# Optimization experiments

Measured on AMD Instinct MI355X. Metric: run time of the kernel, lower is better.

Reference implementation:

```python
import jax, jax.numpy as jnp
import numpy as np

NUM_CLASS = 8192
FEAT_DIM = 512
BATCH = 131072


def setup_inputs() -> dict:
    key = jax.random.key(0)
    k1, k2, k3 = jax.random.split(key, 3)
    batch_samples = jax.random.normal(k1, (BATCH, FEAT_DIM), dtype=jnp.float32)
    class_sums = jnp.zeros((NUM_CLASS, FEAT_DIM), dtype=jnp.float32)
    targets = jax.random.randint(k2, (BATCH,), 0, NUM_CLASS, dtype=jnp.int64)
    idx = jax.random.randint(k3, (BATCH,), 0, BATCH, dtype=jnp.int64)
    return {"batch_samples": batch_samples, "class_sums": class_sums,
            "targets": targets, "idx": idx}


def reference(batch_samples, class_sums, targets, idx):
    # Original forward: for each unique label, class_sums[label] += sum of rows
    # of batch_samples with that label. This is exactly a segment-sum
    # (scatter-add by class label) accumulated into class_sums.
    # idx is unused in the forward math (kept for signature fidelity).
    inc = jax.ops.segment_sum(batch_samples, targets, num_segments=NUM_CLASS)
    return class_sums + inc  # updated class_sums buffer [num_class, feat_dim]
```

## Files before the change

### kernel.cpp

```cpp
#include <hip/hip_runtime.h>
#include <hip/hip_bf16.h>


#define FEAT 512
#define FEAT4 128
#define SCAN_THREADS 256

typedef float f4 __attribute__((ext_vector_type(4)));

__global__ void k_hist(const int4* __restrict__ t4, int* __restrict__ counts,
                       int n4, const int* __restrict__ targets, int batch) {
    int i = blockIdx.x * blockDim.x + threadIdx.x;
    if (i < n4) {
        int4 v = t4[i];
        atomicAdd(&counts[v.x], 1);
        atomicAdd(&counts[v.y], 1);
        atomicAdd(&counts[v.z], 1);
        atomicAdd(&counts[v.w], 1);
    }
    if (i == 0) {
        for (int k = n4 * 4; k < batch; ++k) atomicAdd(&counts[targets[k]], 1);
    }
}

__global__ __launch_bounds__(SCAN_THREADS) void k_scan(const int* __restrict__ counts,
                                                       int* __restrict__ fill,
                                                       int num_class) {
    __shared__ int sh[8192 + 256];
    __shared__ int sums[SCAN_THREADS];
    const int t = threadIdx.x;
    const int bins = num_class / SCAN_THREADS;

    for (int i = t; i < num_class; i += SCAN_THREADS) sh[i + (i >> 5)] = counts[i];
    __syncthreads();

    const int base = t * bins;
    int s = 0;
    for (int i = 0; i < bins; ++i) { int idx = base + i; s += sh[idx + (idx >> 5)]; }
    sums[t] = s;
    __syncthreads();
    for (int off = 1; off < SCAN_THREADS; off <<= 1) {
        int v = (t >= off) ? sums[t - off] : 0;
        __syncthreads();
        sums[t] += v;
        __syncthreads();
    }
    int run = sums[t] - s;
    for (int i = 0; i < bins; ++i) {
        int idx = base + i;
        int c = sh[idx + (idx >> 5)];
        sh[idx + (idx >> 5)] = run;
        run += c;
    }
    __syncthreads();
    for (int i = t; i < num_class; i += SCAN_THREADS) fill[i] = sh[i + (i >> 5)];
}

__global__ void k_scatter(const int4* __restrict__ t4, int* __restrict__ fill,
                          int* __restrict__ rows, int n4,
                          const int* __restrict__ targets, int batch) {
    int i = blockIdx.x * blockDim.x + threadIdx.x;
    if (i < n4) {
        int4 v = t4[i];
        int r = i * 4;
        rows[atomicAdd(&fill[v.x], 1)] = r + 0;
        rows[atomicAdd(&fill[v.y], 1)] = r + 1;
        rows[atomicAdd(&fill[v.z], 1)] = r + 2;
        rows[atomicAdd(&fill[v.w], 1)] = r + 3;
    }
    if (i == 0) {
        for (int k = n4 * 4; k < batch; ++k)
            rows[atomicAdd(&fill[targets[k]], 1)] = k;
    }
}

__global__ __launch_bounds__(128) void k_sum(const f4* __restrict__ batch,
                                             const f4* __restrict__ csums,
                                             const int* __restrict__ fill,
                                             const int* __restrict__ counts,
                                             const int* __restrict__ rows,
                                             f4* __restrict__ out) {
    const int c = blockIdx.x;
    const int t = threadIdx.x;
    const int n = counts[c];
    const int start = fill[c] - n;

    f4 acc = csums[(size_t)c * FEAT4 + t];

    __shared__ int sidx[512];
    for (int chunk = 0; chunk < n; chunk += 512) {
        const int m = min(n - chunk, 512);
        for (int j = t; j < m; j += 128) sidx[j] = rows[start + chunk + j];
        __syncthreads();

        int j = 0;
        for (; j + 8 <= m; j += 8) {
            f4 v0 = __builtin_nontemporal_load(&batch[(size_t)sidx[j + 0] * FEAT4 + t]);
            f4 v1 = __builtin_nontemporal_load(&batch[(size_t)sidx[j + 1] * FEAT4 + t]);
            f4 v2 = __builtin_nontemporal_load(&batch[(size_t)sidx[j + 2] * FEAT4 + t]);
            f4 v3 = __builtin_nontemporal_load(&batch[(size_t)sidx[j + 3] * FEAT4 + t]);
            f4 v4 = __builtin_nontemporal_load(&batch[(size_t)sidx[j + 4] * FEAT4 + t]);
            f4 v5 = __builtin_nontemporal_load(&batch[(size_t)sidx[j + 5] * FEAT4 + t]);
            f4 v6 = __builtin_nontemporal_load(&batch[(size_t)sidx[j + 6] * FEAT4 + t]);
            f4 v7 = __builtin_nontemporal_load(&batch[(size_t)sidx[j + 7] * FEAT4 + t]);
            acc += ((v0 + v1) + (v2 + v3)) + ((v4 + v5) + (v6 + v7));
        }
        for (; j < m; ++j) {
            f4 v = __builtin_nontemporal_load(&batch[(size_t)sidx[j] * FEAT4 + t]);
            acc += v;
        }
        __syncthreads();
    }
    __builtin_nontemporal_store(acc, &out[(size_t)c * FEAT4 + t]);
}

__global__ void k_copy(const float4* __restrict__ src, float4* __restrict__ dst, int n4) {
    int i = blockIdx.x * blockDim.x + threadIdx.x;
    if (i < n4) dst[i] = src[i];
}

__global__ __launch_bounds__(128) void k_atomic(const float4* __restrict__ batch,
                                                const int* __restrict__ targets,
                                                float* __restrict__ out, int batch_n) {
    const int r = blockIdx.x;
    const int t = threadIdx.x;
    if (r >= batch_n) return;
    float4 v = batch[(size_t)r * FEAT4 + t];
    float* o = out + (size_t)targets[r] * FEAT + t * 4;
    atomicAdd(o + 0, v.x);
    atomicAdd(o + 1, v.y);
    atomicAdd(o + 2, v.z);
    atomicAdd(o + 3, v.w);
}

extern "C" void kernel_launch(void* const* d_in, const int* in_sizes, int n_in,
                              void* d_out, int out_size, void* d_ws, size_t ws_size,
                              hipStream_t stream) {
    const float* batch_samples = (const float*)d_in[0];
    const float* class_sums    = (const float*)d_in[1];
    const int*   targets       = (const int*)d_in[2];

    const int batch     = in_sizes[2];
    const int num_class = out_size / FEAT;
    float* out = (float*)d_out;

    const size_t need = (size_t)num_class * 4 * 2 + (size_t)batch * 4;
    if (ws_size >= need && (num_class % SCAN_THREADS) == 0 && num_class <= 8192) {
        int* counts = (int*)d_ws;
        int* fill   = counts + num_class;
        int* rows   = fill + num_class;
        const int n4 = batch / 4;

        (void)hipMemsetAsync(counts, 0, (size_t)num_class * 4, stream);
        k_hist<<<(n4 + 255) / 256, 256, 0, stream>>>((const int4*)targets, counts,
                                                     n4, targets, batch);
        k_scan<<<1, SCAN_THREADS, 0, stream>>>(counts, fill, num_class);
        k_scatter<<<(n4 + 255) / 256, 256, 0, stream>>>((const int4*)targets, fill,
                                                        rows, n4, targets, batch);
        k_sum<<<num_class, 128, 0, stream>>>((const f4*)batch_samples,
                                             (const f4*)class_sums,
                                             fill, counts, rows,
                                             (f4*)out);
    } else {
        const int nv4 = out_size / 4;
        k_copy<<<(nv4 + 255) / 256, 256, 0, stream>>>((const float4*)class_sums,
                                                      (float4*)out, nv4);
        k_atomic<<<batch, 128, 0, stream>>>((const float4*)batch_samples,
                                            targets, out, batch);
    }
}
```

Before: 379.7 us.

## Replace histogram+scan with fixed-capacity per-class buckets and atomic overflow path

Removes the histogram and single-block scan kernels. Row indices are now scattered straight into fixed 128-slot per-class buckets, and any rows past that capacity go to an overflow list. The overflow rows are added afterwards with float atomics in a separate kernel. This cuts two launches and one pass over targets, but it needs a larger workspace and adds an overflow kernel launch that must read the overflow count.

```diff
diff --git a/kernel.cpp b/kernel.cpp
--- a/kernel.cpp
+++ b/kernel.cpp
@@ -4,114 +4,88 @@
 
 #define FEAT 512
 #define FEAT4 128
-#define SCAN_THREADS 256
+#define CAP   128
 
 typedef float f4 __attribute__((ext_vector_type(4)));
 
-__global__ void k_hist(const int4* __restrict__ t4, int* __restrict__ counts,
-                       int n4, const int* __restrict__ targets, int batch) {
-    int i = blockIdx.x * blockDim.x + threadIdx.x;
-    if (i < n4) {
-        int4 v = t4[i];
-        atomicAdd(&counts[v.x], 1);
-        atomicAdd(&counts[v.y], 1);
-        atomicAdd(&counts[v.z], 1);
-        atomicAdd(&counts[v.w], 1);
-    }
-    if (i == 0) {
-        for (int k = n4 * 4; k < batch; ++k) atomicAdd(&counts[targets[k]], 1);
-    }
-}
-
-__global__ __launch_bounds__(SCAN_THREADS) void k_scan(const int* __restrict__ counts,
-                                                       int* __restrict__ fill,
-                                                       int num_class) {
-    __shared__ int sh[8192 + 256];
-    __shared__ int sums[SCAN_THREADS];
-    const int t = threadIdx.x;
-    const int bins = num_class / SCAN_THREADS;
-
-    for (int i = t; i < num_class; i += SCAN_THREADS) sh[i + (i >> 5)] = counts[i];
-    __syncthreads();
-
-    const int base = t * bins;
-    int s = 0;
-    for (int i = 0; i < bins; ++i) { int idx = base + i; s += sh[idx + (idx >> 5)]; }
-    sums[t] = s;
-    __syncthreads();
-    for (int off = 1; off < SCAN_THREADS; off <<= 1) {
-        int v = (t >= off) ? sums[t - off] : 0;
-        __syncthreads();
-        sums[t] += v;
-        __syncthreads();
-    }
-    int run = sums[t] - s;
-    for (int i = 0; i < bins; ++i) {
-        int idx = base + i;
-        int c = sh[idx + (idx >> 5)];
-        sh[idx + (idx >> 5)] = run;
-        run += c;
-    }
-    __syncthreads();
-    for (int i = t; i < num_class; i += SCAN_THREADS) fill[i] = sh[i + (i >> 5)];
+__device__ __forceinline__ void bucket_one(int c, int row, int* __restrict__ fill,
+                                           int* __restrict__ rows_buf,
+                                           int* __restrict__ ovf_cnt,
+                                           int* __restrict__ ovf) {
+    int pos = atomicAdd(&fill[c], 1);
+    if (pos < CAP) rows_buf[c * CAP + pos] = row;
+    else           ovf[atomicAdd(ovf_cnt, 1)] = row;
 }
 
 __global__ void k_scatter(const int4* __restrict__ t4, int* __restrict__ fill,
-                          int* __restrict__ rows, int n4,
+                          int* __restrict__ rows_buf, int* __restrict__ ovf_cnt,
+                          int* __restrict__ ovf, int n4,
                           const int* __restrict__ targets, int batch) {
     int i = blockIdx.x * blockDim.x + threadIdx.x;
     if (i < n4) {
         int4 v = t4[i];
         int r = i * 4;
-        rows[atomicAdd(&fill[v.x], 1)] = r + 0;
-        rows[atomicAdd(&fill[v.y], 1)] = r + 1;
-        rows[atomicAdd(&fill[v.z], 1)] = r + 2;
-        rows[atomicAdd(&fill[v.w], 1)] = r + 3;
+        bucket_one(v.x, r + 0, fill, rows_buf, ovf_cnt, ovf);
+        bucket_one(v.y, r + 1, fill, rows_buf, ovf_cnt, ovf);
+        bucket_one(v.z, r + 2, fill, rows_buf, ovf_cnt, ovf);
+        bucket_one(v.w, r + 3, fill, rows_buf, ovf_cnt, ovf);
     }
     if (i == 0) {
         for (int k = n4 * 4; k < batch; ++k)
-            rows[atomicAdd(&fill[targets[k]], 1)] = k;
+            bucket_one(targets[k], k, fill, rows_buf, ovf_cnt, ovf);
     }
 }
 
 __global__ __launch_bounds__(128) void k_sum(const f4* __restrict__ batch,
                                              const f4* __restrict__ csums,
                                              const int* __restrict__ fill,
-                                             const int* __restrict__ counts,
-                                             const int* __restrict__ rows,
+                                             const int* __restrict__ rows_buf,
                                              f4* __restrict__ out) {
     const int c = blockIdx.x;
     const int t = threadIdx.x;
-    const int n = counts[c];
-    const int start = fill[c] - n;
+    const int n = min(fill[c], CAP);
+
+    __shared__ int sidx[CAP];
+    if (t < n) sidx[t] = rows_buf[c * CAP + t];
+    __syncthreads();
 
     f4 acc = csums[(size_t)c * FEAT4 + t];
 
-    __shared__ int sidx[512];
-    for (int chunk = 0; chunk < n; chunk += 512) {
-        const int m = min(n - chunk, 512);
-        for (int j = t; j < m; j += 128) sidx[j] = rows[start + chunk + j];
-        __syncthreads();
+    int j = 0;
+    for (; j + 8 <= n; j += 8) {
+        f4 v0 = __builtin_nontemporal_load(&batch[(size_t)sidx[j + 0] * FEAT4 + t]);
+        f4 v1 = __builtin_nontemporal_load(&batch[(size_t)sidx[j + 1] * FEAT4 + t]);
+        f4 v2 = __builtin_nontemporal_load(&batch[(size_t)sidx[j + 2] * FEAT4 + t]);
+        f4 v3 = __builtin_nontemporal_load(&batch[(size_t)sidx[j + 3] * FEAT4 + t]);
+        f4 v4 = __builtin_nontemporal_load(&batch[(size_t)sidx[j + 4] * FEAT4 + t]);
+        f4 v5 = __builtin_nontemporal_load(&batch[(size_t)sidx[j + 5] * FEAT4 + t]);
+        f4 v6 = __builtin_nontemporal_load(&batch[(size_t)sidx[j + 6] * FEAT4 + t]);
+        f4 v7 = __builtin_nontemporal_load(&batch[(size_t)sidx[j + 7] * FEAT4 + t]);
+        acc += ((v0 + v1) + (v2 + v3)) + ((v4 + v5) + (v6 + v7));
+    }
+    for (; j < n; ++j)
+        acc += __builtin_nontemporal_load(&batch[(size_t)sidx[j] * FEAT4 + t]);
 
-        int j = 0;
-        for (; j + 8 <= m; j += 8) {
-            f4 v0 = __builtin_nontemporal_load(&batch[(size_t)sidx[j + 0] * FEAT4 + t]);
-            f4 v1 = __builtin_nontemporal_load(&batch[(size_t)sidx[j + 1] * FEAT4 + t]);
-            f4 v2 = __builtin_nontemporal_load(&batch[(size_t)sidx[j + 2] * FEAT4 + t]);
-            f4 v3 = __builtin_nontemporal_load(&batch[(size_t)sidx[j + 3] * FEAT4 + t]);
-            f4 v4 = __builtin_nontemporal_load(&batch[(size_t)sidx[j + 4] * FEAT4 + t]);
-            f4 v5 = __builtin_nontemporal_load(&batch[(size_t)sidx[j + 5] * FEAT4 + t]);
-            f4 v6 = __builtin_nontemporal_load(&batch[(size_t)sidx[j + 6] * FEAT4 + t]);
-            f4 v7 = __builtin_nontemporal_load(&batch[(size_t)sidx[j + 7] * FEAT4 + t]);
-            acc += ((v0 + v1) + (v2 + v3)) + ((v4 + v5) + (v6 + v7));
-        }
-        for (; j < m; ++j) {
-            f4 v = __builtin_nontemporal_load(&batch[(size_t)sidx[j] * FEAT4 + t]);
-            acc += v;
-        }
-        __syncthreads();
+    __builtin_nontemporal_store(acc, &out[(size_t)c * FEAT4 + t]);
+}
+
+__global__ __launch_bounds__(128) void k_ovf(const f4* __restrict__ batch,
+                                             const int* __restrict__ targets,
+                                             const int* __restrict__ ovf_cnt,
+                                             const int* __restrict__ ovf,
+                                             float* __restrict__ out) {
+    const int cnt = *ovf_cnt;
+    const int t = threadIdx.x;
+    for (int e = blockIdx.x; e < cnt; e += gridDim.x) {
+        int row = ovf[e];
+        int c = targets[row];
+        f4 v = batch[(size_t)row * FEAT4 + t];
+        float* o = out + (size_t)c * FEAT + t * 4;
+        atomicAdd(o + 0, v.x);
+        atomicAdd(o + 1, v.y);
+        atomicAdd(o + 2, v.z);
+        atomicAdd(o + 3, v.w);
     }
-    __builtin_nontemporal_store(acc, &out[(size_t)c * FEAT4 + t]);
 }
 
 __global__ void k_copy(const float4* __restrict__ src, float4* __restrict__ dst, int n4) {
@@ -144,23 +118,26 @@
     const int num_class = out_size / FEAT;
     float* out = (float*)d_out;
 
-    const size_t need = (size_t)num_class * 4 * 2 + (size_t)batch * 4;
-    if (ws_size >= need && (num_class % SCAN_THREADS) == 0 && num_class <= 8192) {
-        int* counts = (int*)d_ws;
-        int* fill   = counts + num_class;
-        int* rows   = fill + num_class;
+    const size_t rows_off = ((size_t)num_class + 64) & ~63ull;
+    const size_t ovf_off  = rows_off + (size_t)num_class * CAP;
+    const size_t need     = (ovf_off + (size_t)batch) * 4;
+
+    if (ws_size >= need) {
+        int* fill     = (int*)d_ws;
+        int* ovf_cnt  = fill + num_class;
+        int* rows_buf = fill + rows_off;
+        int* ovf      = fill + ovf_off;
         const int n4 = batch / 4;
 
-        (void)hipMemsetAsync(counts, 0, (size_t)num_class * 4, stream);
-        k_hist<<<(n4 + 255) / 256, 256, 0, stream>>>((const int4*)targets, counts,
-                                                     n4, targets, batch);
-        k_scan<<<1, SCAN_THREADS, 0, stream>>>(counts, fill, num_class);
+        (void)hipMemsetAsync(fill, 0, ((size_t)num_class + 1) * 4, stream);
         k_scatter<<<(n4 + 255) / 256, 256, 0, stream>>>((const int4*)targets, fill,
-                                                        rows, n4, targets, batch);
+                                                        rows_buf, ovf_cnt, ovf,
+                                                        n4, targets, batch);
         k_sum<<<num_class, 128, 0, stream>>>((const f4*)batch_samples,
                                              (const f4*)class_sums,
-                                             fill, counts, rows,
-                                             (f4*)out);
+                                             fill, rows_buf, (f4*)out);
+        k_ovf<<<256, 128, 0, stream>>>((const f4*)batch_samples, targets,
+                                       ovf_cnt, ovf, out);
     } else {
         const int nv4 = out_size / 4;
         k_copy<<<(nv4 + 255) / 256, 256, 0, stream>>>((const float4*)class_sums,
```

Result: no change. 374.7 us (-1.3%).
